# Kernel optimization log

Hardware: AMD Instinct MI355X
Metric: run time of the kernel (lower is better)

## Reference

```python
import jax, jax.numpy as jnp
import numpy as np


def conv2d_nchw(x, w, b, padding):
    # x: [B,Cin,H,W], w: [Cout,Cin,kh,kw]
    y = jax.lax.conv_general_dilated(
        x, w, window_strides=(1, 1), padding=padding,
        dimension_numbers=("NCHW", "OIHW", "NCHW"))
    return y + b[None, :, None, None]


def setup_inputs() -> dict:
    key = jax.random.key(0)
    ks = jax.random.split(key, 8)
    B, C, H, W = 8, 512, 50, 76
    A = 9  # 3 scales x 3 ratios
    base_feat = jax.random.normal(ks[0], (B, C, H, W), dtype=jnp.float32)
    im_info = jnp.tile(jnp.array([800.0, 1216.0, 1.0], jnp.float32), (B, 1))
    gt_boxes = jax.random.uniform(ks[1], (B, 20, 5), dtype=jnp.float32) * 100.0
    num_boxes = jax.random.randint(ks[2], (B,), 1, 20, dtype=jnp.int32)
    # learned parameters (Kaiming-ish small init)
    conv_w = jax.random.normal(ks[3], (512, C, 3, 3), dtype=jnp.float32) * 0.01
    conv_b = jnp.zeros((512,), jnp.float32)
    cls_w = jax.random.normal(ks[4], (2 * A, 512, 1, 1), dtype=jnp.float32) * 0.01
    cls_b = jnp.zeros((2 * A,), jnp.float32)
    bbox_w = jax.random.normal(ks[5], (4 * A, 512, 1, 1), dtype=jnp.float32) * 0.01
    bbox_b = jnp.zeros((4 * A,), jnp.float32)
    return dict(base_feat=base_feat, im_info=im_info, gt_boxes=gt_boxes,
                num_boxes=num_boxes, conv_w=conv_w, conv_b=conv_b,
                cls_w=cls_w, cls_b=cls_b, bbox_w=bbox_w, bbox_b=bbox_b)


def reference(base_feat, im_info, gt_boxes, num_boxes,
              conv_w, conv_b, cls_w, cls_b, bbox_w, bbox_b):
    # RPN_Conv 3x3 + ReLU
    rpn_conv = jax.nn.relu(conv2d_nchw(base_feat, conv_w, conv_b, "SAME"))
    # 1x1 cls head -> [B, 2A, H, W]
    rpn_cls_score = conv2d_nchw(rpn_conv, cls_w, cls_b, "VALID")
    B, C2, H, W = rpn_cls_score.shape
    # _RPN.reshape(x, 2): view as [B, 2, A*H, W], softmax over the 2-way dim
    score_rs = rpn_cls_score.reshape(B, 2, (C2 // 2) * H, W)
    prob_rs = jax.nn.softmax(score_rs, axis=1)
    rpn_cls_prob = prob_rs.reshape(B, C2, H, W)
    # 1x1 bbox head -> [B, 4A, H, W]
    rpn_bbox_pred = conv2d_nchw(rpn_conv, bbox_w, bbox_b, "VALID")
    return rpn_cls_prob, rpn_bbox_pred
```

## Files before the change

kernel.cpp:

```cpp
#include <hip/hip_runtime.h>
#include <hip/hip_bf16.h>


typedef __bf16 bf16_t;
typedef __attribute__((ext_vector_type(8))) __bf16 bf16x8;
typedef __attribute__((ext_vector_type(4))) __bf16 bf16x4;
typedef __attribute__((ext_vector_type(4))) float f32x4;

#define HW 3800
#define NPOS (8 * HW)
#define XP_IMG (52 * 78 * 512)

__device__ __forceinline__ void gload_lds16(const bf16_t* g, char* l) {
  __builtin_amdgcn_global_load_lds(
      (const __attribute__((address_space(1))) unsigned int*)g,
      (__attribute__((address_space(3))) unsigned int*)l, 16, 0, 0);
}

__global__ __launch_bounds__(256) void pad_nhwc(const float* __restrict__ x,
                                                bf16_t* __restrict__ Xp) {
  const int t = threadIdx.x;
  const int blk = blockIdx.x;
  if (blk < 1600) {
    __shared__ __align__(16) bf16_t tile[76][136];
    const int cb = blk & 3;
    int r = blk >> 2;
    const int h = r % 50, b = r / 50;
#pragma unroll
    for (int it = 0; it < 10; ++it) {
      int idx = it * 256 + t;
      if (idx < 2432) {
        int c = idx / 19, w4 = idx - c * 19;
        const float4 v = *(const float4*)(x +
            (((size_t)(b * 512 + cb * 128 + c)) * 50 + h) * 76 + w4 * 4);
        tile[w4 * 4 + 0][c] = (bf16_t)v.x;
        tile[w4 * 4 + 1][c] = (bf16_t)v.y;
        tile[w4 * 4 + 2][c] = (bf16_t)v.z;
        tile[w4 * 4 + 3][c] = (bf16_t)v.w;
      }
    }
    __syncthreads();
#pragma unroll
    for (int it = 0; it < 5; ++it) {
      int idx = it * 256 + t;
      if (idx < 1216) {
        int w = idx >> 4, c8 = idx & 15;
        bf16x8 v = *(const bf16x8*)&tile[w][c8 * 8];
        *(bf16x8*)(Xp + ((size_t)(b * 52 + h + 1) * 78 + (w + 1)) * 512 +
                   cb * 128 + c8 * 8) = v;
      }
    }
  } else {
    const int blk2 = blk - 1600;
    const int b = blk2 >> 1, half = blk2 & 1;
    bf16x8 z;
#pragma unroll
    for (int j = 0; j < 8; ++j) z[j] = (bf16_t)0.f;
#pragma unroll
    for (int it = 0; it < 32; ++it) {
      int idx = it * 256 + t;
      int q = half * 128 + (idx >> 6);
      int c8 = idx & 63;
      int h, w;
      if (q < 78)       { h = 0;           w = q; }
      else if (q < 156) { h = 51;          w = q - 78; }
      else if (q < 206) { h = q - 156 + 1; w = 0; }
      else              { h = q - 206 + 1; w = 77; }
      *(bf16x8*)(Xp + ((size_t)(b * 52 + h) * 78 + w) * 512 + c8 * 8) = z;
    }
  }
}

__global__ __launch_bounds__(256) void wtrans(const float* __restrict__ cw,
                                              bf16_t* __restrict__ Wt) {
  __shared__ bf16_t lw[4608];
  const int t = threadIdx.x;
  const int co = blockIdx.x;
  const float* src = cw + (size_t)co * 4608;
#pragma unroll
  for (int it = 0; it < 18; ++it) {
    int idx = it * 256 + t;
    lw[idx] = (bf16_t)src[idx];
  }
  __syncthreads();
#pragma unroll
  for (int s = 0; s < 9; ++s) {
    int ci = t * 2;
    bf16_t v0 = lw[ci * 9 + s], v1 = lw[(ci + 1) * 9 + s];
    bf16_t* dst = Wt + ((size_t)s * 512 + co) * 512 + ci;
    dst[0] = v0; dst[1] = v1;
  }
}

__global__ __launch_bounds__(256) void whb_build(const float* __restrict__ clsw,
                                                 const float* __restrict__ boxw,
                                                 bf16_t* __restrict__ Whb) {
  int t = blockIdx.x * 256 + threadIdx.x;
  int ci = t & 511; int row = t >> 9;
  float v = 0.f;
  if (row < 18) {
    int a = row >> 1, logit = row & 1;
    v = clsw[(logit * 9 + a) * 512 + ci];
  } else if (row < 54) {
    v = boxw[(row - 18) * 512 + ci];
  }
  Whb[(size_t)row * 512 + ci] = (bf16_t)v;
}

__global__ __launch_bounds__(512, 2) void conv3x3(const bf16_t* __restrict__ Xp,
                                                  const bf16_t* __restrict__ Wt,
                                                  const float* __restrict__ convb,
                                                  bf16_t* __restrict__ rc2) {
  __shared__ __align__(16) char smem[131072];
  const int tid = threadIdx.x;
  const int lane = tid & 63;
  const int wv = tid >> 6;
  const int wm = wv >> 2;
  const int wn = wv & 3;
  const int lm = lane & 15, lg = lane >> 4;

  const int raw = blockIdx.x;
  const int wg = (raw & 7) * 30 + (raw >> 3);
  const int b = wg / 30;
  const int rem = wg - b * 30;
  const int co_base = (rem & 1) * 256;
  const int pos_base = (rem >> 1) * 256;
  const bf16_t* XpB = Xp + (size_t)b * XP_IMG;

  int aSrc[2][2], aDst[2][2];
#pragma unroll
  for (int mh = 0; mh < 2; ++mh)
#pragma unroll
    for (int i = 0; i < 2; ++i) {
      int d = i * 512 + tid;
      int rl = d >> 3, p = d & 7;
      int rp = ((rl >> 6) << 7) + mh * 64 + (rl & 63);
      int c = p ^ (rp & 7);
      aSrc[mh][i] = (co_base + rp) * 512 + c * 8;
      aDst[mh][i] = rp * 128 + p * 16;
    }
  int bSpa[2][2], bCc[2][2], bDst[2][2];
#pragma unroll
  for (int f = 0; f < 2; ++f)
#pragma unroll
    for (int i = 0; i < 2; ++i) {
      int d = i * 512 + tid;
      int rl = d >> 3, p = d & 7;
      int rp = ((rl >> 5) << 6) + f * 32 + (rl & 31);
      int c = p ^ (rp & 7);
      int m = pos_base + rp; if (m > HW - 1) m = HW - 1;
      bSpa[f][i] = (m / 76) * 78 + (m - (m / 76) * 76);
      bCc[f][i] = c * 8;
      bDst[f][i] = 32768 + rp * 128 + p * 16;
    }

  const int koff0 = (lg ^ (lm & 7)) << 4;
  const int koff1 = ((4 + lg) ^ (lm & 7)) << 4;
  int aOff[8], bOff[4];
#pragma unroll
  for (int m = 0; m < 8; ++m) aOff[m] = (wm * 128 + m * 16 + lm) * 128;
#pragma unroll
  for (int n = 0; n < 4; ++n) bOff[n] = 32768 + (wn * 64 + n * 16 + lm) * 128;

  f32x4 acc[8][4];
#pragma unroll
  for (int i = 0; i < 8; ++i)
#pragma unroll
    for (int j = 0; j < 4; ++j) acc[i][j] = (f32x4){0.f, 0.f, 0.f, 0.f};

  bf16x8 ar[4][2], br[4][2];

#define STAGE_A(KT, BUF, MH) {                                                  \
    const int s_ = (KT) >> 3, cb_ = (KT) & 7;                                   \
    const bf16_t* p_ = Wt + (size_t)s_ * 262144 + cb_ * 64;                     \
    _Pragma("unroll")                                                           \
    for (int i_ = 0; i_ < 2; ++i_)                                              \
      gload_lds16(p_ + aSrc[MH][i_], (BUF) + aDst[MH][i_]);                     \
  }
#define STAGE_B(KT, BUF, F) {                                                   \
    const int s_ = (KT) >> 3, cb_ = (KT) & 7;                                   \
    const int sp_ = (s_ / 3) * 78 + (s_ - (s_ / 3) * 3);                        \
    _Pragma("unroll")                                                           \
    for (int i_ = 0; i_ < 2; ++i_)                                              \
      gload_lds16(XpB + (size_t)(bSpa[F][i_] + sp_) * 512 + bCc[F][i_] +        \
                      cb_ * 64,                                                 \
                  (BUF) + bDst[F][i_]);                                         \
  }
#define RD_A(BASE, MLO)                                                         \
    _Pragma("unroll")                                                           \
    for (int m_ = 0; m_ < 4; ++m_) {                                            \
      ar[m_][0] = *(const bf16x8*)((BASE) + aOff[(MLO) + m_] + koff0);          \
      ar[m_][1] = *(const bf16x8*)((BASE) + aOff[(MLO) + m_] + koff1);          \
    }
#define RD_B(BASE, NLO)                                                         \
    _Pragma("unroll")                                                           \
    for (int n_ = 0; n_ < 2; ++n_) {                                            \
      br[(NLO) + n_][0] = *(const bf16x8*)((BASE) + bOff[(NLO) + n_] + koff0);  \
      br[(NLO) + n_][1] = *(const bf16x8*)((BASE) + bOff[(NLO) + n_] + koff1);  \
    }
#define MF_Q(AM, NLO)                                                           \
    _Pragma("unroll")                                                           \
    for (int m_ = 0; m_ < 4; ++m_)                                              \
      _Pragma("unroll")                                                         \
      for (int n_ = 0; n_ < 2; ++n_)                                            \
        _Pragma("unroll")                                                       \
        for (int k_ = 0; k_ < 2; ++k_)                                          \
          acc[(AM) + m_][(NLO) + n_] = __builtin_amdgcn_mfma_f32_16x16x32_bf16( \
              ar[m_][k_], br[(NLO) + n_][k_], acc[(AM) + m_][(NLO) + n_], 0, 0, 0);
#define SYNC_MFMA                                                               \
    __builtin_amdgcn_s_barrier();                                               \
    asm volatile("s_waitcnt lgkmcnt(0)" ::: "memory");                          \
    __builtin_amdgcn_sched_barrier(0);
#define VM6 asm volatile("s_waitcnt vmcnt(6)" ::: "memory");
#define VM0 asm volatile("s_waitcnt vmcnt(0)" ::: "memory");
#define PRIO1 __builtin_amdgcn_s_setprio(1);
#define PRIO0 __builtin_amdgcn_s_setprio(0);
#define ENDP __builtin_amdgcn_s_barrier();

#define DO_ITER(E, STG, P4W, P8W) {                                             \
    char* bE = smem;                                                            \
    char* bO = smem + 65536;                                                    \
     RD_B(bE, 0) RD_A(bE, 0) STAGE_A((E) + 1, bO, 1)                    \
      SYNC_MFMA PRIO1 MF_Q(0, 0) PRIO0 ENDP                                     \
     RD_B(bE, 2) if (STG) STAGE_B((E) + 2, bE, 0)                       \
      SYNC_MFMA PRIO1 MF_Q(0, 2) PRIO0 ENDP                                     \
     RD_A(bE, 4) if (STG) STAGE_A((E) + 2, bE, 0)                       \
      SYNC_MFMA PRIO1 MF_Q(4, 2) PRIO0 ENDP                                     \
     if (STG) STAGE_B((E) + 2, bE, 1)                                   \
      SYNC_MFMA PRIO1 MF_Q(4, 0) PRIO0 P4W ENDP                                 \
     RD_B(bO, 0) RD_A(bO, 0) if (STG) STAGE_A((E) + 2, bE, 1)           \
      SYNC_MFMA PRIO1 MF_Q(0, 0) PRIO0 ENDP                                     \
     RD_B(bO, 2) if (STG) STAGE_B((E) + 3, bO, 0)                       \
      SYNC_MFMA PRIO1 MF_Q(0, 2) PRIO0 ENDP                                     \
     RD_A(bO, 4) if (STG) STAGE_A((E) + 3, bO, 0)                       \
      SYNC_MFMA PRIO1 MF_Q(4, 2) PRIO0 ENDP                                     \
     if (STG) STAGE_B((E) + 3, bO, 1)                                   \
      SYNC_MFMA PRIO1 MF_Q(4, 0) PRIO0 P8W ENDP                                 \
  }

  STAGE_B(0, smem, 0) STAGE_A(0, smem, 0) STAGE_B(0, smem, 1) STAGE_A(0, smem, 1)
  STAGE_B(1, smem + 65536, 0) STAGE_A(1, smem + 65536, 0) STAGE_B(1, smem + 65536, 1)
  VM6
  __builtin_amdgcn_s_barrier();
  __builtin_amdgcn_sched_barrier(0);

  for (int it = 0; it < 35; ++it) {
    DO_ITER(2 * it, true, VM6, VM6)
  }
  DO_ITER(70, false, VM0, )

#undef DO_ITER
#undef STAGE_A
#undef STAGE_B
#undef RD_A
#undef RD_B
#undef MF_Q
#undef SYNC_MFMA
#undef VM6
#undef VM0
#undef PRIO1
#undef PRIO0
#undef ENDP

  const size_t outRow = (size_t)b * HW;
#pragma unroll
  for (int m = 0; m < 8; ++m) {
    const int co = co_base + wm * 128 + m * 16 + lg * 4;
    const float4 bias = *(const float4*)(convb + co);
#pragma unroll
    for (int n = 0; n < 4; ++n) {
      const int pos = pos_base + wn * 64 + n * 16 + lm;
      if (pos < HW) {
        bf16x4 v;
        float z0 = acc[m][n][0] + bias.x; v[0] = (bf16_t)(z0 > 0.f ? z0 : 0.f);
        float z1 = acc[m][n][1] + bias.y; v[1] = (bf16_t)(z1 > 0.f ? z1 : 0.f);
        float z2 = acc[m][n][2] + bias.z; v[2] = (bf16_t)(z2 > 0.f ? z2 : 0.f);
        float z3 = acc[m][n][3] + bias.w; v[3] = (bf16_t)(z3 > 0.f ? z3 : 0.f);
        *(bf16x4*)(rc2 + (outRow + pos) * 512 + co) = v;
      }
    }
  }
}

__global__ __launch_bounds__(256) void heads_mfma(const bf16_t* __restrict__ rc2,
                                                  const bf16_t* __restrict__ Whb,
                                                  const float* __restrict__ clsb,
                                                  const float* __restrict__ boxb,
                                                  float* __restrict__ out) {
  __shared__ __align__(16) char smem[24576];
  const int t = threadIdx.x, lane = t & 63, wv = t >> 6;
  const int lm = lane & 15, lg = lane >> 4, lx = lane & 7;
  const int pos_base = blockIdx.x * 128;

  int aSrc[2], bSrc[4];
#pragma unroll
  for (int i = 0; i < 2; ++i) {
    int d = i * 256 + t;
    int r = d >> 3, p = d & 7, c = p ^ (r & 7);
    aSrc[i] = r * 512 + c * 8;
  }
#pragma unroll
  for (int i = 0; i < 4; ++i) {
    int d = i * 256 + t;
    int r = d >> 3, p = d & 7, c = p ^ (r & 7);
    int pg = pos_base + r; if (pg > NPOS - 1) pg = NPOS - 1;
    bSrc[i] = pg * 512 + c * 8;
  }

  f32x4 acc[4][2];
#pragma unroll
  for (int i = 0; i < 4; ++i)
#pragma unroll
    for (int j = 0; j < 2; ++j) acc[i][j] = (f32x4){0.f, 0.f, 0.f, 0.f};

  for (int cb = 0; cb < 8; ++cb) {
    __syncthreads();
#pragma unroll
    for (int i = 0; i < 2; ++i) {
      int d = i * 256 + t;
      gload_lds16(Whb + aSrc[i] + cb * 64, &smem[d * 16]);
    }
#pragma unroll
    for (int i = 0; i < 4; ++i) {
      int d = i * 256 + t;
      gload_lds16(rc2 + (size_t)bSrc[i] + cb * 64, &smem[8192 + d * 16]);
    }
    __syncthreads();
#pragma unroll
    for (int ks = 0; ks < 2; ++ks) {
      const int koff = ((ks * 4 + lg) ^ lx) << 4;
      bf16x8 af[4], bfr[2];
#pragma unroll
      for (int f = 0; f < 4; ++f)
        af[f] = *(const bf16x8*)&smem[(f * 16 + lm) * 128 + koff];
#pragma unroll
      for (int f = 0; f < 2; ++f)
        bfr[f] = *(const bf16x8*)&smem[8192 + (wv * 32 + f * 16 + lm) * 128 + koff];
#pragma unroll
      for (int fa = 0; fa < 4; ++fa)
#pragma unroll
        for (int fb = 0; fb < 2; ++fb)
          acc[fa][fb] = __builtin_amdgcn_mfma_f32_16x16x32_bf16(
              af[fa], bfr[fb], acc[fa][fb], 0, 0, 0);
    }
  }

  float* boxOut = out + (size_t)8 * 18 * HW;
#pragma unroll
  for (int fb = 0; fb < 2; ++fb) {
    const int pg = pos_base + wv * 32 + fb * 16 + lm;
    if (pg < NPOS) {
      const int b = pg / HW;
      const int m = pg - b * HW;
#pragma unroll
      for (int fa = 0; fa < 4; ++fa) {
        const int base = fa * 16 + lg * 4;
#pragma unroll
        for (int pr = 0; pr < 2; ++pr) {
          const int row0 = base + pr * 2;
          const float v0 = acc[fa][fb][pr * 2];
          const float v1 = acc[fa][fb][pr * 2 + 1];
          if (row0 < 18) {
            const int a = row0 >> 1;
            const float s0 = v0 + clsb[a];
            const float s1 = v1 + clsb[9 + a];
            const float mx = fmaxf(s0, s1);
            const float e0 = expf(s0 - mx), e1 = expf(s1 - mx);
            const float inv = 1.0f / (e0 + e1);
            out[((size_t)(b * 18 + a)) * HW + m] = e0 * inv;
            out[((size_t)(b * 18 + 9 + a)) * HW + m] = e1 * inv;
          } else if (row0 < 54) {
            const int c0 = row0 - 18;
            boxOut[((size_t)(b * 36 + c0)) * HW + m] = v0 + boxb[c0];
            boxOut[((size_t)(b * 36 + c0 + 1)) * HW + m] = v1 + boxb[c0 + 1];
          }
        }
      }
    }
  }
}

extern "C" void kernel_launch(void* const* d_in, const int* in_sizes, int n_in,
                              void* d_out, int out_size, void* d_ws, size_t ws_size,
                              hipStream_t stream) {
  (void)in_sizes; (void)n_in; (void)out_size; (void)ws_size;
  const float* base_feat = (const float*)d_in[0];
  const float* conv_w = (const float*)d_in[4];
  const float* conv_b = (const float*)d_in[5];
  const float* cls_w  = (const float*)d_in[6];
  const float* cls_b  = (const float*)d_in[7];
  const float* bbox_w = (const float*)d_in[8];
  const float* bbox_b = (const float*)d_in[9];

  char* ws = (char*)d_ws;
  bf16_t* Xp  = (bf16_t*)(ws);
  bf16_t* Wt  = (bf16_t*)(ws + 33226752);
  bf16_t* rc2 = (bf16_t*)(ws + 37945344);
  bf16_t* Whb = (bf16_t*)(ws + 69074944);

  hipLaunchKernelGGL(pad_nhwc,   dim3(1616), dim3(256), 0, stream, base_feat, Xp);
  hipLaunchKernelGGL(wtrans,     dim3(512),  dim3(256), 0, stream, conv_w, Wt);
  hipLaunchKernelGGL(whb_build,  dim3(128),  dim3(256), 0, stream, cls_w, bbox_w, Whb);
  hipLaunchKernelGGL(conv3x3,    dim3(240),  dim3(512), 0, stream, Xp, Wt, conv_b, rc2);
  hipLaunchKernelGGL(heads_mfma, dim3(238),  dim3(256), 0, stream, rc2, Whb, cls_b, bbox_b,
                     (float*)d_out);
}
```

Measured before the change: 160.5 us.

## Restructure conv GEMM main loop into four-phase tile schedule with split register buffers

Rewrites the double-buffered MFMA main loop so that each K tile runs four MFMA quadrants with separate register sets for the low and high A halves and the two B halves. All four B fragments are read at the start of a tile, and the next tile's low A half is prefetched during the last quadrant. The per-phase barrier-plus-lgkmcnt(0) waits become bare sched_barriers, and global-to-LDS staging is regrouped into larger batches with vmcnt(8) waits. The aim is to cut barrier and LDS-wait stalls between phases and overlap LDS reads with MFMA work, at the cost of more live registers and a reliance on the compiler to insert correct LDS wait counts.

```diff
diff --git a/kernel.cpp b/kernel.cpp
--- a/kernel.cpp
+++ b/kernel.cpp
@@ -168,7 +168,7 @@
 #pragma unroll
     for (int j = 0; j < 4; ++j) acc[i][j] = (f32x4){0.f, 0.f, 0.f, 0.f};
 
-  bf16x8 ar[4][2], br[4][2];
+  bf16x8 ar_lo[4][2], ar_hi[4][2], br01[2][2], br23[2][2];
 
 #define STAGE_A(KT, BUF, MH) {                                                  \
     const int s_ = (KT) >> 3, cb_ = (KT) & 7;                                   \
@@ -186,81 +186,96 @@
                       cb_ * 64,                                                 \
                   (BUF) + bDst[F][i_]);                                         \
   }
-#define RD_A(BASE, MLO)                                                         \
+#define RD_ALO(BASE)                                                            \
     _Pragma("unroll")                                                           \
     for (int m_ = 0; m_ < 4; ++m_) {                                            \
-      ar[m_][0] = *(const bf16x8*)((BASE) + aOff[(MLO) + m_] + koff0);          \
-      ar[m_][1] = *(const bf16x8*)((BASE) + aOff[(MLO) + m_] + koff1);          \
-    }
-#define RD_B(BASE, NLO)                                                         \
+      ar_lo[m_][0] = *(const bf16x8*)((BASE) + aOff[m_] + koff0);               \
+      ar_lo[m_][1] = *(const bf16x8*)((BASE) + aOff[m_] + koff1);               \
+    }
+#define RD_AHI(BASE)                                                            \
+    _Pragma("unroll")                                                           \
+    for (int m_ = 0; m_ < 4; ++m_) {                                            \
+      ar_hi[m_][0] = *(const bf16x8*)((BASE) + aOff[4 + m_] + koff0);           \
+      ar_hi[m_][1] = *(const bf16x8*)((BASE) + aOff[4 + m_] + koff1);           \
+    }
+#define RD_B01(BASE)                                                            \
     _Pragma("unroll")                                                           \
     for (int n_ = 0; n_ < 2; ++n_) {                                            \
-      br[(NLO) + n_][0] = *(const bf16x8*)((BASE) + bOff[(NLO) + n_] + koff0);  \
-      br[(NLO) + n_][1] = *(const bf16x8*)((BASE) + bOff[(NLO) + n_] + koff1);  \
-    }
-#define MF_Q(AM, NLO)                                                           \
+      br01[n_][0] = *(const bf16x8*)((BASE) + bOff[n_] + koff0);                \
+      br01[n_][1] = *(const bf16x8*)((BASE) + bOff[n_] + koff1);                \
+    }
+#define RD_B23(BASE)                                                            \
+    _Pragma("unroll")                                                           \
+    for (int n_ = 0; n_ < 2; ++n_) {                                            \
+      br23[n_][0] = *(const bf16x8*)((BASE) + bOff[2 + n_] + koff0);            \
+      br23[n_][1] = *(const bf16x8*)((BASE) + bOff[2 + n_] + koff1);            \
+    }
+#define MQ(AARR, AOFS, BARR, NOFS)                                              \
     _Pragma("unroll")                                                           \
     for (int m_ = 0; m_ < 4; ++m_)                                              \
       _Pragma("unroll")                                                         \
       for (int n_ = 0; n_ < 2; ++n_)                                            \
         _Pragma("unroll")                                                       \
         for (int k_ = 0; k_ < 2; ++k_)                                          \
-          acc[(AM) + m_][(NLO) + n_] = __builtin_amdgcn_mfma_f32_16x16x32_bf16( \
-              ar[m_][k_], br[(NLO) + n_][k_], acc[(AM) + m_][(NLO) + n_], 0, 0, 0);
-#define SYNC_MFMA                                                               \
-    __builtin_amdgcn_s_barrier();                                               \
-    asm volatile("s_waitcnt lgkmcnt(0)" ::: "memory");                          \
-    __builtin_amdgcn_sched_barrier(0);
-#define VM6 asm volatile("s_waitcnt vmcnt(6)" ::: "memory");
-#define VM0 asm volatile("s_waitcnt vmcnt(0)" ::: "memory");
+          acc[(AOFS) + m_][(NOFS) + n_] =                                       \
+              __builtin_amdgcn_mfma_f32_16x16x32_bf16(                          \
+                  AARR[m_][k_], BARR[n_][k_], acc[(AOFS) + m_][(NOFS) + n_],    \
+                  0, 0, 0);
+#define SCB __builtin_amdgcn_sched_barrier(0);
+#define BAR __builtin_amdgcn_s_barrier();
 #define PRIO1 __builtin_amdgcn_s_setprio(1);
 #define PRIO0 __builtin_amdgcn_s_setprio(0);
-#define ENDP __builtin_amdgcn_s_barrier();
-
-#define DO_ITER(E, STG, P4W, P8W) {                                             \
-    char* bE = smem;                                                            \
-    char* bO = smem + 65536;                                                    \
-     RD_B(bE, 0) RD_A(bE, 0) STAGE_A((E) + 1, bO, 1)                    \
-      SYNC_MFMA PRIO1 MF_Q(0, 0) PRIO0 ENDP                                     \
-     RD_B(bE, 2) if (STG) STAGE_B((E) + 2, bE, 0)                       \
-      SYNC_MFMA PRIO1 MF_Q(0, 2) PRIO0 ENDP                                     \
-     RD_A(bE, 4) if (STG) STAGE_A((E) + 2, bE, 0)                       \
-      SYNC_MFMA PRIO1 MF_Q(4, 2) PRIO0 ENDP                                     \
-     if (STG) STAGE_B((E) + 2, bE, 1)                                   \
-      SYNC_MFMA PRIO1 MF_Q(4, 0) PRIO0 P4W ENDP                                 \
-     RD_B(bO, 0) RD_A(bO, 0) if (STG) STAGE_A((E) + 2, bE, 1)           \
-      SYNC_MFMA PRIO1 MF_Q(0, 0) PRIO0 ENDP                                     \
-     RD_B(bO, 2) if (STG) STAGE_B((E) + 3, bO, 0)                       \
-      SYNC_MFMA PRIO1 MF_Q(0, 2) PRIO0 ENDP                                     \
-     RD_A(bO, 4) if (STG) STAGE_A((E) + 3, bO, 0)                       \
-      SYNC_MFMA PRIO1 MF_Q(4, 2) PRIO0 ENDP                                     \
-     if (STG) STAGE_B((E) + 3, bO, 1)                                   \
-      SYNC_MFMA PRIO1 MF_Q(4, 0) PRIO0 P8W ENDP                                 \
-  }
-
-  STAGE_B(0, smem, 0) STAGE_A(0, smem, 0) STAGE_B(0, smem, 1) STAGE_A(0, smem, 1)
-  STAGE_B(1, smem + 65536, 0) STAGE_A(1, smem + 65536, 0) STAGE_B(1, smem + 65536, 1)
-  VM6
-  __builtin_amdgcn_s_barrier();
-  __builtin_amdgcn_sched_barrier(0);
+#define VM8 asm volatile("s_waitcnt vmcnt(8)" ::: "memory");
+#define VM0 asm volatile("s_waitcnt vmcnt(0)" ::: "memory");
+#define VMNONE
+
+#define DO_TILE(TT, BUF, NBUF, STG, WC, LDN) {                                  \
+                    \
+    RD_B01(BUF) RD_B23(BUF)                                                     \
+    SCB PRIO1 MQ(ar_lo, 0, br01, 0) PRIO0 BAR                                   \
+                                     \
+    RD_AHI(BUF)                                                                 \
+    if (STG) { STAGE_A((TT) + 2, BUF, 0) STAGE_B((TT) + 2, BUF, 0)              \
+               STAGE_B((TT) + 2, BUF, 1) }                                      \
+    SCB PRIO1 MQ(ar_lo, 0, br23, 2) PRIO0 BAR                                   \
+                        \
+    if (STG) STAGE_A((TT) + 2, BUF, 1)                                          \
+    SCB PRIO1 MQ(ar_hi, 4, br23, 2) PRIO0 WC BAR                                \
+                \
+    if (LDN) RD_ALO(NBUF)                                                       \
+    SCB PRIO1 MQ(ar_hi, 4, br01, 0) PRIO0 BAR                                   \
+  }
+
+  STAGE_A(0, smem, 0) STAGE_A(0, smem, 1) STAGE_B(0, smem, 0) STAGE_B(0, smem, 1)
+  STAGE_A(1, smem + 65536, 0) STAGE_A(1, smem + 65536, 1)
+  STAGE_B(1, smem + 65536, 0) STAGE_B(1, smem + 65536, 1)
+  VM8
+  BAR
+  RD_ALO(smem)
 
   for (int it = 0; it < 35; ++it) {
-    DO_ITER(2 * it, true, VM6, VM6)
-  }
-  DO_ITER(70, false, VM0, )
-
-#undef DO_ITER
+    const int E = 2 * it;
+    DO_TILE(E,     smem,         smem + 65536, true, VM8, true)
+    DO_TILE(E + 1, smem + 65536, smem,         true, VM8, true)
+  }
+  DO_TILE(70, smem,         smem + 65536, false, VM0, true)
+  DO_TILE(71, smem + 65536, smem,         false, VMNONE, false)
+
+#undef DO_TILE
 #undef STAGE_A
 #undef STAGE_B
-#undef RD_A
-#undef RD_B
-#undef MF_Q
-#undef SYNC_MFMA
-#undef VM6
-#undef VM0
+#undef RD_ALO
+#undef RD_AHI
+#undef RD_B01
+#undef RD_B23
+#undef MQ
+#undef SCB
+#undef BAR
 #undef PRIO1
 #undef PRIO0
-#undef ENDP
+#undef VM8
+#undef VM0
+#undef VMNONE
 
   const size_t outRow = (size_t)b * HW;
 #pragma unroll
```

New measurement: 470.9 us. 2.93x slower.
